# Optimization experiments

Hardware: AMD Instinct MI355X
Metric: run time of the kernel (lower is better)

## Reference

```python
import jax, jax.numpy as jnp
import numpy as np

IGST = 10      # ghost-cell width (module-level constant in the source)
EPS = 0.01     # tol passed to NeuralODE -> runge_kutta eps
W_SCALE = 0.05 # keep the learned stencil contractive over 100 steps


def cal_boundry(u):
    # Replace the IGST ghost cells on each side with the nearest interior value.
    m, n, l = u.shape
    left = jnp.broadcast_to(u[:, :, IGST:IGST + 1], (m, n, IGST))
    right = jnp.broadcast_to(u[:, :, -IGST - 1:-IGST], (m, n, IGST))
    return jnp.concatenate([left, u[:, :, IGST:-IGST], right], axis=2)


def stencil_f(z, W):
    # func: learned 1D stencil = same-padded conv over the spatial axis.
    # z: [m, n, l], W: [n_out, n_in, k]
    return jax.lax.conv_general_dilated(
        z, W, window_strides=(1,), padding='SAME',
        dimension_numbers=('NCH', 'OIH', 'NCH'))


def setup_inputs() -> dict:
    key = jax.random.key(0)
    k1, k2 = jax.random.split(key)
    z0 = jax.random.normal(k1, (32, 16, 8192), dtype=jnp.float32)
    W = jax.random.normal(k2, (16, 16, 5), dtype=jnp.float32) * W_SCALE
    return {'z0': z0, 'W': W, 't1_t0': 1}


def reference(z0, W, t1_t0):
    # SSP-RK3 (Shu-Osher) explicit time stepping with ghost-cell BCs.
    n_steps = int(round(t1_t0 / EPS))
    h = t1_t0 / n_steps

    def step(z, _):
        k1 = cal_boundry(z + h * stencil_f(z, W))
        k2 = cal_boundry(0.75 * z + 0.25 * k1 + 0.25 * h * stencil_f(k1, W))
        z_new = cal_boundry(z / 3.0 + 2.0 * k2 / 3.0 + 2.0 * h * stencil_f(k2, W) / 3.0)
        return z_new, None

    z, _ = jax.lax.scan(step, z0, None, length=n_steps)
    return z
```

## Files before the change

### kernel.cpp

```cpp
#include <hip/hip_runtime.h>


#define NCH    16
#define LL     8192
#define TX     128
#define NBX    64
#define NB     32
#define NSTEPS 100
#define SPK    5
#define NKER   (NSTEPS / SPK)

#define RAD    30
#define NCHUNK 31
#define ISLAB  190

#define WCOLS  96
#define DWIN   1072
#define NROWS  592
#define NMT    37
#define NKC    34
#define XSTR   1096

typedef __bf16 bf16x8 __attribute__((ext_vector_type(8)));
typedef __bf16 bf16x4 __attribute__((ext_vector_type(4)));
typedef float  f32x4  __attribute__((ext_vector_type(4)));

__device__ __align__(16) float g_G [ 5*256];
__device__ __align__(16) float g_G2[ 9*256];
__device__ __align__(16) float g_Tp[13*256];
__device__ __align__(16) float g_T2[25*256];
__device__ __align__(16) float g_T3[37*256];
__device__ __align__(16) float g_T4[49*256];
__device__ __align__(16) float g_T5[61*256];
__device__ __align__(16) __bf16 g_Sfrag[NCHUNK*64*8];
__device__ __align__(16) float g_CL[(size_t)NROWS*DWIN];
__device__ __align__(16) float g_CR[(size_t)NROWS*DWIN];
__device__ __align__(16) __bf16 g_Cpack[2][NMT][NKC][512];

__global__ void build_G(const float* __restrict__ W, const int* __restrict__ tptr) {
  const float h = (float)(*tptr) / (float)NSTEPS;
  const int o = threadIdx.x >> 4, i = threadIdx.x & 15;
#pragma unroll
  for (int k = 0; k < 5; ++k)
    g_G[k*256 + o*16 + i] = h * W[o*80 + i*5 + k];
}

__global__ void compose_k(int mode) {
  const float* A; int ra; const float* B; int rb; float* C;
  switch (mode) {
    case 0:  A = g_G;  ra = 2;  B = g_G;  rb = 2; C = g_G2; break;
    case 1:  A = g_G2; ra = 4;  B = g_G;  rb = 2; C = g_Tp; break;
    case 2:  A = g_Tp; ra = 6;  B = g_Tp; rb = 6; C = g_T2; break;
    case 3:  A = g_T2; ra = 12; B = g_Tp; rb = 6; C = g_T3; break;
    case 4:  A = g_T3; ra = 18; B = g_Tp; rb = 6; C = g_T4; break;
    default: A = g_T4; ra = 24; B = g_Tp; rb = 6; C = g_T5; break;
  }
  const int rc = ra + rb;
  const int d = (int)blockIdx.x - rc;
  const int o = threadIdx.x >> 4, i = threadIdx.x & 15;
  float acc = 0.f;
  for (int a = -ra; a <= ra; ++a) {
    const int b = d - a;
    if (b < -rb || b > rb) continue;
    const float* Am = A + (a+ra)*256 + o*16;
    const float* Bm = B + (b+rb)*256 + i;
#pragma unroll
    for (int j = 0; j < 16; ++j) acc += Am[j] * Bm[j*16];
  }
  C[(size_t)blockIdx.x*256 + o*16 + i] = acc;
}

__global__ void build_Tp() {
  const int o = threadIdx.x >> 4, i = threadIdx.x & 15;
#pragma unroll
  for (int k = 0; k < 13; ++k) {
    const int d = k - 6;
    float v = g_Tp[k*256 + o*16 + i] * (1.f/6.f);
    if (d >= -4 && d <= 4) v += 0.5f * g_G2[(d+4)*256 + o*16 + i];
    if (d >= -2 && d <= 2) v += g_G[(d+2)*256 + o*16 + i];
    g_Tp[k*256 + o*16 + i] = v;
  }
}

__device__ __forceinline__ float padread(const float* M, int r, int d, int oi) {
  return (d >= -r && d <= r) ? M[(d+r)*256 + oi] : 0.f;
}

__global__ void pack_S() {
  const int c = blockIdx.x;
  const int lane = threadIdx.x & 63;
  const int jj = (threadIdx.x >> 6) * 2;
  const int gg = lane >> 4, n = lane & 15;
  const int k = 2*c + (gg >> 1);
  const int d = k - RAD;
#pragma unroll
  for (int u = 0; u < 2; ++u) {
    const int j = jj + u;
    const int i = (gg & 1)*8 + j;
    const int oi = n*16 + i;
    float v = 0.f;
    if (k <= 60) {
      v = 5.f  * padread(g_Tp,  6, d, oi)
        + 10.f * padread(g_T2, 12, d, oi)
        + 10.f * padread(g_T3, 18, d, oi)
        + 5.f  * padread(g_T4, 24, d, oi)
        +        padread(g_T5, 30, d, oi);
    }
    g_Sfrag[((size_t)c*64 + lane)*8 + j] = (__bf16)v;
  }
}

__global__ void pack_C() {
  const int mt = blockIdx.x, e = blockIdx.y;
  const float* __restrict__ C = e ? g_CR : g_CL;
  __bf16* __restrict__ P = &g_Cpack[e][mt][0][0];
  for (int idx = threadIdx.x; idx < NKC * 512; idx += 256) {
    const int kc = idx >> 9, q = idx & 511;
    const int ln = q >> 3, j = q & 7;
    const int k = kc * 32 + (ln >> 4) * 8 + j;
    const int row = mt * 16 + (ln & 15);
    P[idx] = (__bf16)((k < DWIN) ? C[(size_t)row * DWIN + k] : 0.f);
  }
}

__device__ __forceinline__ int ldsIdx(int col, int ch) {
  return col * NCH + (ch ^ ((col & 4) << 1));
}

__device__ __forceinline__ bf16x8 mkA(const float* __restrict__ W, int c, int g, int n) {
  const int kk = c * 2 + (g >> 1);
  bf16x8 a;
#pragma unroll
  for (int j = 0; j < 8; ++j) {
    const int i = (g & 1) * 8 + j;
    a[j] = (__bf16)((kk < 5) ? W[n * (NCH * 5) + i * 5 + kk] : 0.0f);
  }
  return a;
}

__global__ __launch_bounds__(384)
void edge_evolve(const float* __restrict__ W, const int* __restrict__ tptr) {
  __shared__ __align__(16) __bf16 ES[2][WCOLS * NCH];
  const int j = blockIdx.x, e = blockIdx.y;
  const float h = (float)(*tptr) / (float)NSTEPS;
  const int tid = threadIdx.x, lane = tid & 63, wv = tid >> 6;
  const int g = lane >> 4, n = lane & 15;
  const int t = wv, mycol = 16 * t + n;
  const int cwj = (e ? 29 : 0) + (j >> 4), chj = j & 15;

  const bf16x8 af0 = mkA(W, 0, g, n);
  const bf16x8 af1 = mkA(W, 1, g, n);
  const bf16x8 af2 = mkA(W, 2, g, n);

  const int hot = ldsIdx(cwj, chj);
  for (int q = tid; q < WCOLS * NCH; q += 384)
    ES[0][q] = (__bf16)(q == hot ? 1.f : 0.f);

  f32x4 kz = {0.f, 0.f, 0.f, 0.f};
  if (mycol == cwj && g == (chj >> 2)) kz[chj & 3] = 1.f;
  f32x4 kf = {0.f, 0.f, 0.f, 0.f};
  __syncthreads();

  const float c13 = 1.0f / 3.0f, c23 = 2.0f / 3.0f;
  int rb = 0;
#pragma unroll 1
  for (int sp = 0; sp < SPK; ++sp) {
#pragma unroll 1
    for (int st = 0; st < 3; ++st) {
      const float az  = (st == 0) ? 1.0f : (st == 1) ? 0.75f : c13;
      const float ak  = (st == 0) ? 0.0f : (st == 1) ? 0.25f : c23;
      const float agh = (st == 0) ? h    : (st == 1) ? 0.25f*h : c23*h;
      const __bf16* RS = ES[rb];
      __bf16* WS = ES[rb ^ 1];
      f32x4 acc = {0.f, 0.f, 0.f, 0.f};
#pragma unroll
      for (int c = 0; c < 3; ++c) {
        const int kk = c * 2 + (g >> 1);
        int s = mycol + kk - 2;
        s = min(max(s, 0), WCOLS - 1);
        const bf16x8 bfrag = *(const bf16x8*)(&RS[ldsIdx(s, (g & 1) * 8)]);
        const bf16x8 a = (c == 0) ? af0 : (c == 1) ? af1 : af2;
        acc = __builtin_amdgcn_mfma_f32_16x16x32_bf16(a, bfrag, acc, 0, 0, 0);
      }
      f32x4 v;
#pragma unroll
      for (int r = 0; r < 4; ++r) v[r] = az * kz[r] + ak * kf[r] + agh * acc[r];
      if (e == 0 && t == 0) {
#pragma unroll
        for (int r = 0; r < 4; ++r) {
          const float sv = __shfl(v[r], (lane & 48) | 10, 64);
          if (n < 10) v[r] = sv;
        }
      }
      if (e == 1 && t == 5) {
#pragma unroll
        for (int r = 0; r < 4; ++r) {
          const float sv = __shfl(v[r], (lane & 48) | 5, 64);
          if (n > 5) v[r] = sv;
        }
      }
      kf = v;
      if (st == 2) kz = v;
      bf16x4 bv = { (__bf16)v[0], (__bf16)v[1], (__bf16)v[2], (__bf16)v[3] };
      *(bf16x4*)(&WS[ldsIdx(mycol, g * 4)]) = bv;
      __syncthreads();
      rb ^= 1;
    }
  }

  if (e == 0) {
    if (mycol <= 36) {
      const int rowb = mycol * 16 + g * 4;
#pragma unroll
      for (int r = 0; r < 4; ++r) {
        const float id = (mycol == cwj && (g * 4 + r) == chj) ? 1.f : 0.f;
        g_CL[(size_t)(rowb + r) * DWIN + j] = kz[r] - id;
      }
    }
  } else {
    if (mycol >= 59) {
      const int rowb = (mycol - 59) * 16 + g * 4;
#pragma unroll
      for (int r = 0; r < 4; ++r) {
        const float id = (mycol == cwj && (g * 4 + r) == chj) ? 1.f : 0.f;
        g_CR[(size_t)(rowb + r) * DWIN + j] = kz[r] - id;
      }
    }
  }
}

__global__ __launch_bounds__(256) void transpose_kernel(const float* __restrict__ in,
                                                        float* __restrict__ out) {
  const int b = blockIdx.y;
  const int x = blockIdx.x * 256 + threadIdx.x;
  const float* __restrict__ ib = in + (size_t)b * NCH * LL;
  float* __restrict__ ob = out + (size_t)b * NCH * LL;
  float v[NCH];
#pragma unroll
  for (int c = 0; c < NCH; ++c) v[c] = ib[c * LL + x];
#pragma unroll
  for (int c = 0; c < NCH; c += 4)
    *(float4*)(ob + (size_t)x * NCH + c) = make_float4(v[c], v[c+1], v[c+2], v[c+3]);
}

__global__ __launch_bounds__(256)
void multistep_kernel(
    const float* __restrict__ zin,
    float* __restrict__ zout,
    const int* __restrict__ tptr, int finalKer)
{
  __shared__ __align__(16) char SMEM[16 * XSTR * 2];

  const int b = blockIdx.y, bx = blockIdx.x;
  const int tid = threadIdx.x, lane = tid & 63, wv = tid >> 6;
  const int g = lane >> 4, n = lane & 15;

  if (bx < NBX) {
    __bf16* __restrict__ ISL = (__bf16*)SMEM;
    const float* __restrict__ zb = zin + (size_t)b * NCH * LL;
    float* __restrict__ ob = zout + (size_t)b * NCH * LL;
    const int x0 = bx * TX;
    const bool leftE = (bx == 0), rightE = (bx == NBX - 1);

    for (int q = tid; q < ISLAB * 4; q += 256) {
      const int s = q >> 2, cg = (q & 3) * 4;
      int gx = x0 - RAD + s;
      gx = min(max(gx, 0), LL - 1);
      const float4 v = *(const float4*)(zb + (size_t)gx * NCH + cg);
      bf16x4 bv = { (__bf16)v.x, (__bf16)v.y, (__bf16)v.z, (__bf16)v.w };
      *(bf16x4*)(&ISL[ldsIdx(s, cg)]) = bv;
    }

    const int o0 = 16 * wv + n;
    const f32x4 kz0 = *(const f32x4*)(zb + (size_t)(x0 + o0) * NCH + g * 4);
    const f32x4 kz1 = *(const f32x4*)(zb + (size_t)(x0 + o0 + 64) * NCH + g * 4);
    __syncthreads();

    const int p = g >> 1, hsel = g & 1;
    f32x4 acc0 = {0.f,0.f,0.f,0.f}, acc1 = acc0;
    const __bf16* Af = g_Sfrag + (size_t)lane * 8;
    int col0 = o0 + p;
#pragma unroll
    for (int c = 0; c < NCHUNK; ++c) {
      const bf16x8 a = *(const bf16x8*)(Af + (size_t)c * 512);
      const int xr = ((((col0 >> 2) & 1) ^ hsel) << 4);
      const bf16x8 b0 = *(const bf16x8*)((const char*)ISL + col0 * 32 + xr);
      const bf16x8 b1 = *(const bf16x8*)((const char*)ISL + (col0 + 64) * 32 + xr);
      acc0 = __builtin_amdgcn_mfma_f32_16x16x32_bf16(a, b0, acc0, 0, 0, 0);
      acc1 = __builtin_amdgcn_mfma_f32_16x16x32_bf16(a, b1, acc1, 0, 0, 0);
      col0 += 2;
    }

    f32x4 v0, v1;
#pragma unroll
    for (int r = 0; r < 4; ++r) { v0[r] = kz0[r] + acc0[r]; v1[r] = kz1[r] + acc1[r]; }

    const bool st0 = !(leftE && o0 <= 36);
    const bool st1 = !(rightE && o0 >= 27);
    if (!finalKer) {
      if (st0) *(f32x4*)(ob + (size_t)(x0 + o0) * NCH + g * 4) = v0;
      if (st1) *(f32x4*)(ob + (size_t)(x0 + o0 + 64) * NCH + g * 4) = v1;
    } else {
#pragma unroll
      for (int r = 0; r < 4; ++r) {
        if (st0) ob[(size_t)(g * 4 + r) * LL + (x0 + o0)] = v0[r];
        if (st1) ob[(size_t)(g * 4 + r) * LL + (x0 + o0 + 64)] = v1[r];
      }
    }
  } else {
    const int rid = b;
    const int side = rid & 1, bhalf = (rid >> 1) & 1, mseg = rid >> 2;
    __bf16* __restrict__ XL = (__bf16*)SMEM;
    const size_t woff = side ? (size_t)(LL - 67) * NCH : 0;

    for (int q = tid; q < 16 * 268; q += 256) {
      const int bb = q / 268, c4 = q % 268;
      const f32x4 v = *(const f32x4*)(zin + (size_t)(bhalf*16 + bb) * NCH * LL
                                      + woff + c4 * 4);
      bf16x4 bv = { (__bf16)v[0], (__bf16)v[1], (__bf16)v[2], (__bf16)v[3] };
      *(bf16x4*)(&XL[bb * XSTR + c4 * 4]) = bv;
    }
    for (int q = tid; q < 16 * 16; q += 256)
      XL[(q >> 4) * XSTR + 1072 + (q & 15)] = (__bf16)0.f;
    __syncthreads();

    const int q = mseg * 4 + wv;
    const int mt0 = q, mt1 = q + 32;
    const bool has1 = (mt1 < NMT);
    f32x4 acc0 = {0.f,0.f,0.f,0.f}, acc1 = acc0;
    const __bf16* __restrict__ Cp = &g_Cpack[side][0][0][0];
    const __bf16* __restrict__ Xr = &XL[n * XSTR + g * 8];

#pragma unroll 2
    for (int kc = 0; kc < NKC; ++kc) {
      const bf16x8 a = *(const bf16x8*)(Xr + kc * 32);
      const bf16x8 b0 = *(const bf16x8*)(Cp + ((size_t)mt0 * NKC + kc) * 512 + lane * 8);
      acc0 = __builtin_amdgcn_mfma_f32_16x16x32_bf16(a, b0, acc0, 0, 0, 0);
      if (has1) {
        const bf16x8 b1 = *(const bf16x8*)(Cp + ((size_t)mt1 * NKC + kc) * 512 + lane * 8);
        acc1 = __builtin_amdgcn_mfma_f32_16x16x32_bf16(a, b1, acc1, 0, 0, 0);
      }
    }

#pragma unroll
    for (int i = 0; i < 2; ++i) {
      if (i == 1 && !has1) break;
      const int mt = i ? mt1 : mt0;
      const f32x4 acc = i ? acc1 : acc0;
      const int x = side ? (LL - 37 + mt) : mt;
#pragma unroll
      for (int r = 0; r < 4; ++r) {
        const int bb = bhalf * 16 + 4 * g + r;
        const size_t base = (size_t)bb * NCH * LL;
        const float ov = zin[base + (size_t)x * NCH + n] + acc[r];
        if (!finalKer) zout[base + (size_t)x * NCH + n] = ov;
        else           zout[base + (size_t)n * LL + x] = ov;
      }
    }
  }
}

extern "C" void kernel_launch(void* const* d_in, const int* in_sizes, int n_in,
                              void* d_out, int out_size, void* d_ws, size_t ws_size,
                              hipStream_t stream) {
  const float* z0 = (const float*)d_in[0];
  const float* W  = (const float*)d_in[1];
  const int*   t  = (const int*)d_in[2];

  float* Q = (float*)d_out;
  float* P = (float*)d_ws;

  build_G<<<dim3(1), dim3(256), 0, stream>>>(W, t);
  compose_k<<<dim3( 9), dim3(256), 0, stream>>>(0);
  compose_k<<<dim3(13), dim3(256), 0, stream>>>(1);
  build_Tp<<<dim3(1), dim3(256), 0, stream>>>();
  compose_k<<<dim3(25), dim3(256), 0, stream>>>(2);
  compose_k<<<dim3(37), dim3(256), 0, stream>>>(3);
  compose_k<<<dim3(49), dim3(256), 0, stream>>>(4);
  compose_k<<<dim3(61), dim3(256), 0, stream>>>(5);
  pack_S<<<dim3(NCHUNK), dim3(256), 0, stream>>>();

  edge_evolve<<<dim3(DWIN, 2), dim3(384), 0, stream>>>(W, t);
  pack_C<<<dim3(NMT, 2), dim3(256), 0, stream>>>();

  dim3 block(256);
  transpose_kernel<<<dim3(32, NB), block, 0, stream>>>(z0, Q);

  dim3 mgrid(NBX + 1, NB);
  for (int k = 1; k <= NKER; ++k) {
    if (k & 1) multistep_kernel<<<mgrid, block, 0, stream>>>(Q, P, t, 0);
    else       multistep_kernel<<<mgrid, block, 0, stream>>>(P, Q, t, k == NKER);
  }
}
```

Before: 789.2 us.

## Split edge-correction blocks finer and run edge_evolve as a single barrier-free wave

The boundary-correction blocks in multistep_kernel now handle 8 batches each instead of 16, using twice as many blocks and half the shared memory. The aim is to shorten the tail that these long serial MFMA chains add to every launch, at the cost of zero-padded MFMA rows and extra global reads of C. edge_evolve is restructured to use one wave that loops over the six column tiles and keeps its state in LDS, which removes the per-stage block barriers.

```diff
diff --git a/kernel.cpp b/kernel.cpp
--- a/kernel.cpp
+++ b/kernel.cpp
@@ -138,14 +138,15 @@
   return a;
 }
 
-__global__ __launch_bounds__(384)
+__global__ __launch_bounds__(64)
 void edge_evolve(const float* __restrict__ W, const int* __restrict__ tptr) {
   __shared__ __align__(16) __bf16 ES[2][WCOLS * NCH];
+  __shared__ __align__(16) float  KZ[WCOLS * NCH];
+  __shared__ __align__(16) float  KF[WCOLS * NCH];
   const int j = blockIdx.x, e = blockIdx.y;
   const float h = (float)(*tptr) / (float)NSTEPS;
-  const int tid = threadIdx.x, lane = tid & 63, wv = tid >> 6;
+  const int lane = threadIdx.x;
   const int g = lane >> 4, n = lane & 15;
-  const int t = wv, mycol = 16 * t + n;
   const int cwj = (e ? 29 : 0) + (j >> 4), chj = j & 15;
 
   const bf16x8 af0 = mkA(W, 0, g, n);
@@ -153,13 +154,12 @@
   const bf16x8 af2 = mkA(W, 2, g, n);
 
   const int hot = ldsIdx(cwj, chj);
-  for (int q = tid; q < WCOLS * NCH; q += 384)
+  const int hotz = cwj * 16 + chj;
+  for (int q = lane; q < WCOLS * NCH; q += 64) {
     ES[0][q] = (__bf16)(q == hot ? 1.f : 0.f);
-
-  f32x4 kz = {0.f, 0.f, 0.f, 0.f};
-  if (mycol == cwj && g == (chj >> 2)) kz[chj & 3] = 1.f;
-  f32x4 kf = {0.f, 0.f, 0.f, 0.f};
-  __syncthreads();
+    KZ[q] = (q == hotz) ? 1.f : 0.f;
+    KF[q] = 0.f;
+  }
 
   const float c13 = 1.0f / 3.0f, c23 = 2.0f / 3.0f;
   int rb = 0;
@@ -172,59 +172,58 @@
       const float agh = (st == 0) ? h    : (st == 1) ? 0.25f*h : c23*h;
       const __bf16* RS = ES[rb];
       __bf16* WS = ES[rb ^ 1];
-      f32x4 acc = {0.f, 0.f, 0.f, 0.f};
-#pragma unroll
-      for (int c = 0; c < 3; ++c) {
-        const int kk = c * 2 + (g >> 1);
-        int s = mycol + kk - 2;
-        s = min(max(s, 0), WCOLS - 1);
-        const bf16x8 bfrag = *(const bf16x8*)(&RS[ldsIdx(s, (g & 1) * 8)]);
-        const bf16x8 a = (c == 0) ? af0 : (c == 1) ? af1 : af2;
-        acc = __builtin_amdgcn_mfma_f32_16x16x32_bf16(a, bfrag, acc, 0, 0, 0);
+#pragma unroll
+      for (int t = 0; t < 6; ++t) {
+        const int mycol = 16 * t + n;
+        const f32x4 kz = *(const f32x4*)(&KZ[mycol * 16 + g * 4]);
+        const f32x4 kf = *(const f32x4*)(&KF[mycol * 16 + g * 4]);
+        f32x4 acc = {0.f, 0.f, 0.f, 0.f};
+#pragma unroll
+        for (int c = 0; c < 3; ++c) {
+          const int kk = c * 2 + (g >> 1);
+          int s = mycol + kk - 2;
+          s = min(max(s, 0), WCOLS - 1);
+          const bf16x8 bfrag = *(const bf16x8*)(&RS[ldsIdx(s, (g & 1) * 8)]);
+          const bf16x8 a = (c == 0) ? af0 : (c == 1) ? af1 : af2;
+          acc = __builtin_amdgcn_mfma_f32_16x16x32_bf16(a, bfrag, acc, 0, 0, 0);
+        }
+        f32x4 v;
+#pragma unroll
+        for (int r = 0; r < 4; ++r) v[r] = az * kz[r] + ak * kf[r] + agh * acc[r];
+        if (e == 0 && t == 0) {
+#pragma unroll
+          for (int r = 0; r < 4; ++r) {
+            const float sv = __shfl(v[r], (lane & 48) | 10, 64);
+            if (n < 10) v[r] = sv;
+          }
+        }
+        if (e == 1 && t == 5) {
+#pragma unroll
+          for (int r = 0; r < 4; ++r) {
+            const float sv = __shfl(v[r], (lane & 48) | 5, 64);
+            if (n > 5) v[r] = sv;
+          }
+        }
+        *(f32x4*)(&KF[mycol * 16 + g * 4]) = v;
+        if (st == 2) *(f32x4*)(&KZ[mycol * 16 + g * 4]) = v;
+        bf16x4 bv = { (__bf16)v[0], (__bf16)v[1], (__bf16)v[2], (__bf16)v[3] };
+        *(bf16x4*)(&WS[ldsIdx(mycol, g * 4)]) = bv;
       }
-      f32x4 v;
-#pragma unroll
-      for (int r = 0; r < 4; ++r) v[r] = az * kz[r] + ak * kf[r] + agh * acc[r];
-      if (e == 0 && t == 0) {
-#pragma unroll
-        for (int r = 0; r < 4; ++r) {
-          const float sv = __shfl(v[r], (lane & 48) | 10, 64);
-          if (n < 10) v[r] = sv;
-        }
-      }
-      if (e == 1 && t == 5) {
-#pragma unroll
-        for (int r = 0; r < 4; ++r) {
-          const float sv = __shfl(v[r], (lane & 48) | 5, 64);
-          if (n > 5) v[r] = sv;
-        }
-      }
-      kf = v;
-      if (st == 2) kz = v;
-      bf16x4 bv = { (__bf16)v[0], (__bf16)v[1], (__bf16)v[2], (__bf16)v[3] };
-      *(bf16x4*)(&WS[ldsIdx(mycol, g * 4)]) = bv;
-      __syncthreads();
       rb ^= 1;
     }
   }
 
   if (e == 0) {
-    if (mycol <= 36) {
-      const int rowb = mycol * 16 + g * 4;
-#pragma unroll
-      for (int r = 0; r < 4; ++r) {
-        const float id = (mycol == cwj && (g * 4 + r) == chj) ? 1.f : 0.f;
-        g_CL[(size_t)(rowb + r) * DWIN + j] = kz[r] - id;
-      }
+    for (int idx = lane; idx < NROWS; idx += 64) {
+      const int col = idx >> 4, ch = idx & 15;
+      const float id = (col == cwj && ch == chj) ? 1.f : 0.f;
+      g_CL[(size_t)idx * DWIN + j] = KZ[col * 16 + ch] - id;
     }
   } else {
-    if (mycol >= 59) {
-      const int rowb = (mycol - 59) * 16 + g * 4;
-#pragma unroll
-      for (int r = 0; r < 4; ++r) {
-        const float id = (mycol == cwj && (g * 4 + r) == chj) ? 1.f : 0.f;
-        g_CR[(size_t)(rowb + r) * DWIN + j] = kz[r] - id;
-      }
+    for (int idx = lane; idx < NROWS; idx += 64) {
+      const int col = 59 + (idx >> 4), ch = idx & 15;
+      const float id = (col == cwj && ch == chj) ? 1.f : 0.f;
+      g_CR[(size_t)idx * DWIN + j] = KZ[col * 16 + ch] - id;
     }
   }
 }
@@ -249,7 +248,7 @@
     float* __restrict__ zout,
     const int* __restrict__ tptr, int finalKer)
 {
-  __shared__ __align__(16) char SMEM[16 * XSTR * 2];
+  __shared__ __align__(16) char SMEM[8 * XSTR * 2];
 
   const int b = blockIdx.y, bx = blockIdx.x;
   const int tid = threadIdx.x, lane = tid & 63, wv = tid >> 6;
@@ -308,32 +307,37 @@
       }
     }
   } else {
-    const int rid = b;
-    const int side = rid & 1, bhalf = (rid >> 1) & 1, mseg = rid >> 2;
+    const int rid = (bx - NBX) * NB + b;
+    const int side = rid & 1, bgroup = (rid >> 1) & 3, mseg = rid >> 3;
     __bf16* __restrict__ XL = (__bf16*)SMEM;
     const size_t woff = side ? (size_t)(LL - 67) * NCH : 0;
 
-    for (int q = tid; q < 16 * 268; q += 256) {
+    for (int q = tid; q < 8 * 268; q += 256) {
       const int bb = q / 268, c4 = q % 268;
-      const f32x4 v = *(const f32x4*)(zin + (size_t)(bhalf*16 + bb) * NCH * LL
+      const f32x4 v = *(const f32x4*)(zin + (size_t)(bgroup*8 + bb) * NCH * LL
                                       + woff + c4 * 4);
       bf16x4 bv = { (__bf16)v[0], (__bf16)v[1], (__bf16)v[2], (__bf16)v[3] };
       *(bf16x4*)(&XL[bb * XSTR + c4 * 4]) = bv;
     }
-    for (int q = tid; q < 16 * 16; q += 256)
-      XL[(q >> 4) * XSTR + 1072 + (q & 15)] = (__bf16)0.f;
+    if (tid < 8 * 24)
+      XL[(tid / 24) * XSTR + 1072 + (tid % 24)] = (__bf16)0.f;
     __syncthreads();
 
-    const int q = mseg * 4 + wv;
-    const int mt0 = q, mt1 = q + 32;
-    const bool has1 = (mt1 < NMT);
+    const int mt0 = mseg + 8 * wv;
+    const int mt1 = mseg + 32;
+    const bool has1 = (wv == 0 && mt1 < NMT);
     f32x4 acc0 = {0.f,0.f,0.f,0.f}, acc1 = acc0;
     const __bf16* __restrict__ Cp = &g_Cpack[side][0][0][0];
-    const __bf16* __restrict__ Xr = &XL[n * XSTR + g * 8];
+    const __bf16* __restrict__ Xr = &XL[(n & 7) * XSTR + g * 8];
 
 #pragma unroll 2
     for (int kc = 0; kc < NKC; ++kc) {
-      const bf16x8 a = *(const bf16x8*)(Xr + kc * 32);
+      bf16x8 a;
+      if (n < 8) a = *(const bf16x8*)(Xr + kc * 32);
+      else {
+#pragma unroll
+        for (int j = 0; j < 8; ++j) a[j] = (__bf16)0.f;
+      }
       const bf16x8 b0 = *(const bf16x8*)(Cp + ((size_t)mt0 * NKC + kc) * 512 + lane * 8);
       acc0 = __builtin_amdgcn_mfma_f32_16x16x32_bf16(a, b0, acc0, 0, 0, 0);
       if (has1) {
@@ -348,13 +352,15 @@
       const int mt = i ? mt1 : mt0;
       const f32x4 acc = i ? acc1 : acc0;
       const int x = side ? (LL - 37 + mt) : mt;
-#pragma unroll
-      for (int r = 0; r < 4; ++r) {
-        const int bb = bhalf * 16 + 4 * g + r;
-        const size_t base = (size_t)bb * NCH * LL;
-        const float ov = zin[base + (size_t)x * NCH + n] + acc[r];
-        if (!finalKer) zout[base + (size_t)x * NCH + n] = ov;
-        else           zout[base + (size_t)n * LL + x] = ov;
+      if (g < 2) {
+#pragma unroll
+        for (int r = 0; r < 4; ++r) {
+          const int bb = bgroup * 8 + 4 * g + r;
+          const size_t base = (size_t)bb * NCH * LL;
+          const float ov = zin[base + (size_t)x * NCH + n] + acc[r];
+          if (!finalKer) zout[base + (size_t)x * NCH + n] = ov;
+          else           zout[base + (size_t)n * LL + x] = ov;
+        }
       }
     }
   }
@@ -380,13 +386,13 @@
   compose_k<<<dim3(61), dim3(256), 0, stream>>>(5);
   pack_S<<<dim3(NCHUNK), dim3(256), 0, stream>>>();
 
-  edge_evolve<<<dim3(DWIN, 2), dim3(384), 0, stream>>>(W, t);
+  edge_evolve<<<dim3(DWIN, 2), dim3(64), 0, stream>>>(W, t);
   pack_C<<<dim3(NMT, 2), dim3(256), 0, stream>>>();
 
   dim3 block(256);
   transpose_kernel<<<dim3(32, NB), block, 0, stream>>>(z0, Q);
 
-  dim3 mgrid(NBX + 1, NB);
+  dim3 mgrid(NBX + 2, NB);
   for (int k = 1; k <= NKER; ++k) {
     if (k & 1) multistep_kernel<<<mgrid, block, 0, stream>>>(Q, P, t, 0);
     else       multistep_kernel<<<mgrid, block, 0, stream>>>(P, Q, t, k == NKER);
```

New measurement: 813.2 us. +3.0%, slower.
